# Performance work log

Hardware: AMD Instinct MI355X
Metric: run time of the kernel (lower is better)

## Reference

```python
import jax, jax.numpy as jnp
import numpy as np

N = 20000   # num_nodes
R = 32      # num_relations
H = 64      # hidden_size
C = 8       # num_classes
E = 640000  # num_edges


def setup_inputs() -> dict:
    key = jax.random.key(0)
    k = jax.random.split(key, 8)
    edge_index = jax.random.randint(k[0], (2, E), 0, N, dtype=jnp.int64)
    edge_type = jnp.sort(jax.random.randint(k[1], (E,), 0, R, dtype=jnp.int64))
    # offsets per relation into the sorted edge list (R+1 entries)
    tensor_slice = jnp.searchsorted(edge_type, jnp.arange(R + 1)).astype(jnp.int64)
    # conv1: x=None => weight is a per-relation node-embedding table [R, N, H]
    W1 = jax.random.normal(k[2], (R, N, H), dtype=jnp.float32) * (1.0 / np.sqrt(N))
    root1 = jax.random.normal(k[3], (N, H), dtype=jnp.float32) * (1.0 / np.sqrt(N))
    bias1 = jnp.zeros((H,), dtype=jnp.float32)
    W2 = jax.random.normal(k[4], (R, H, C), dtype=jnp.float32) * (1.0 / np.sqrt(H))
    root2 = jax.random.normal(k[5], (H, C), dtype=jnp.float32) * (1.0 / np.sqrt(H))
    bias2 = jnp.zeros((C,), dtype=jnp.float32)
    return {"edge_index": edge_index, "edge_type": edge_type, "tensor_slice": tensor_slice,
            "W1": W1, "root1": root1, "bias1": bias1,
            "W2": W2, "root2": root2, "bias2": bias2}


def reference(edge_index, edge_type, tensor_slice, W1, root1, bias1, W2, root2, bias2):
    src, dst = edge_index[0], edge_index[1]
    # ---- conv1 (x = None): message for edge e is row W1[edge_type[e], src[e]]
    msg1 = W1[edge_type, src]                                   # [E, H] gather
    h = jax.ops.segment_sum(msg1, dst, num_segments=N)          # scatter-add (aggr='add')
    h = h + root1 + bias1                                       # root term = root1[node] since x=None
    h = jax.nn.relu(h)
    # ---- conv2: transform all nodes under every relation once, then gather per edge
    h_rel = jnp.einsum('nh,rhc->rnc', h, W2)                    # [R, N, C]
    msg2 = h_rel[edge_type, src]                                # [E, C] gather
    out = jax.ops.segment_sum(msg2, dst, num_segments=N)        # [N, C]
    out = out + h @ root2 + bias2
    return jax.nn.log_softmax(out, axis=1)
```

## Files before the change

### kernel.cpp

```cpp
#include <hip/hip_runtime.h>
#include <math.h>

#define NN 20000
#define RR 32
#define HH 64
#define CC 8
#define EE 640000
#define CAP 128
#define RT 8

__global__ __launch_bounds__(256) void k_zero(int* __restrict__ cnt) {
    int i = blockIdx.x * 256 + threadIdx.x;
    if (i < NN) cnt[i] = 0;
}

__global__ __launch_bounds__(256) void k_scatter(const int* __restrict__ ei,
                                                 const int* __restrict__ et,
                                                 int* __restrict__ cnt,
                                                 unsigned* __restrict__ pk2) {
    int e = (blockIdx.x * 256 + threadIdx.x) * 4;
    if (e >= EE) return;
    int4 sv = *(const int4*)(ei + e);
    int4 dv = *(const int4*)(ei + EE + e);
    int4 rv = *(const int4*)(et + e);
    int s;
    s = atomicAdd(&cnt[dv.x], 1); pk2[((size_t)dv.x << 7) + s] = (unsigned)sv.x | ((unsigned)rv.x << 15);
    s = atomicAdd(&cnt[dv.y], 1); pk2[((size_t)dv.y << 7) + s] = (unsigned)sv.y | ((unsigned)rv.y << 15);
    s = atomicAdd(&cnt[dv.z], 1); pk2[((size_t)dv.z << 7) + s] = (unsigned)sv.z | ((unsigned)rv.z << 15);
    s = atomicAdd(&cnt[dv.w], 1); pk2[((size_t)dv.w << 7) + s] = (unsigned)sv.w | ((unsigned)rv.w << 15);
}

__global__ __launch_bounds__(256) void k_gather1(const unsigned* __restrict__ pk2,
                                                 const int* __restrict__ cnt,
                                                 const float* __restrict__ W1,
                                                 const float* __restrict__ root1,
                                                 const float* __restrict__ bias1,
                                                 const float* __restrict__ root2,
                                                 float* __restrict__ h,
                                                 float* __restrict__ outr) {
    int wid = (blockIdx.x * 256 + threadIdx.x) >> 6;
    int lane = threadIdx.x & 63;
    if (wid >= NN) return;
    const int eg = lane >> 4;
    const int q  = lane & 15;
    float4 acc4 = make_float4(0.f, 0.f, 0.f, 0.f);
    int beg = wid << 7;
    int end = beg + cnt[wid];
    int i = beg;
    for (; i + 16 <= end; i += 16) {
        unsigned p0 = pk2[i + eg], p1 = pk2[i + 4 + eg];
        unsigned p2 = pk2[i + 8 + eg], p3 = pk2[i + 12 + eg];
        float4 w0 = *((const float4*)(W1 + ((size_t)(p0 >> 15) * NN + (p0 & 0x7fffu)) * HH) + q);
        float4 w1 = *((const float4*)(W1 + ((size_t)(p1 >> 15) * NN + (p1 & 0x7fffu)) * HH) + q);
        float4 w2 = *((const float4*)(W1 + ((size_t)(p2 >> 15) * NN + (p2 & 0x7fffu)) * HH) + q);
        float4 w3 = *((const float4*)(W1 + ((size_t)(p3 >> 15) * NN + (p3 & 0x7fffu)) * HH) + q);
        acc4.x += (w0.x + w1.x) + (w2.x + w3.x);
        acc4.y += (w0.y + w1.y) + (w2.y + w3.y);
        acc4.z += (w0.z + w1.z) + (w2.z + w3.z);
        acc4.w += (w0.w + w1.w) + (w2.w + w3.w);
    }
    for (; i + 4 <= end; i += 4) {
        unsigned p = pk2[i + eg];
        float4 w = *((const float4*)(W1 + ((size_t)(p >> 15) * NN + (p & 0x7fffu)) * HH) + q);
        acc4.x += w.x; acc4.y += w.y; acc4.z += w.z; acc4.w += w.w;
    }
    acc4.x += __shfl_xor(acc4.x, 16); acc4.y += __shfl_xor(acc4.y, 16);
    acc4.z += __shfl_xor(acc4.z, 16); acc4.w += __shfl_xor(acc4.w, 16);
    acc4.x += __shfl_xor(acc4.x, 32); acc4.y += __shfl_xor(acc4.y, 32);
    acc4.z += __shfl_xor(acc4.z, 32); acc4.w += __shfl_xor(acc4.w, 32);
    int sl = lane >> 2;
    float cx = __shfl(acc4.x, sl), cy = __shfl(acc4.y, sl);
    float cz = __shfl(acc4.z, sl), cw = __shfl(acc4.w, sl);
    int comp = lane & 3;
    float acc = cx;
    if (comp == 1) acc = cy;
    if (comp == 2) acc = cz;
    if (comp == 3) acc = cw;
    for (; i < end; ++i) {
        unsigned p = pk2[i];
        acc += W1[((size_t)(p >> 15) * NN + (p & 0x7fffu)) * HH + lane];
    }
    acc += root1[(size_t)wid * HH + lane] + bias1[lane];
    float hv = fmaxf(acc, 0.0f);
    h[(size_t)wid * HH + lane] = hv;
    float4 ra = *(const float4*)(root2 + lane * CC);
    float4 rb = *(const float4*)(root2 + lane * CC + 4);
    float a0 = hv * ra.x, a1 = hv * ra.y, a2 = hv * ra.z, a3 = hv * ra.w;
    float a4 = hv * rb.x, a5 = hv * rb.y, a6 = hv * rb.z, a7 = hv * rb.w;
    #pragma unroll
    for (int m = 1; m < 8; m <<= 1) {
        a0 += __shfl_xor(a0, m); a1 += __shfl_xor(a1, m);
        a2 += __shfl_xor(a2, m); a3 += __shfl_xor(a3, m);
        a4 += __shfl_xor(a4, m); a5 += __shfl_xor(a5, m);
        a6 += __shfl_xor(a6, m); a7 += __shfl_xor(a7, m);
    }
    int c = lane & 7;
    float v = a0;
    if (c == 1) v = a1;  if (c == 2) v = a2;  if (c == 3) v = a3;
    if (c == 4) v = a4;  if (c == 5) v = a5;  if (c == 6) v = a6;
    if (c == 7) v = a7;
    v += __shfl_xor(v, 8);
    v += __shfl_xor(v, 16);
    v += __shfl_xor(v, 32);
    if (lane < 8) outr[(size_t)wid * CC + lane] = v;
}

__global__ __launch_bounds__(256) void k_hrel(const float* __restrict__ h,
                                              const float* __restrict__ W2,
                                              float* __restrict__ hrel) {
    __shared__ float w2s[RT * HH * CC];
    int r0 = blockIdx.y * RT;
    int tid = threadIdx.x;
    #pragma unroll
    for (int u = 0; u < RT * HH * CC / 256; u++)
        w2s[u * 256 + tid] = W2[(size_t)r0 * HH * CC + u * 256 + tid];
    __syncthreads();
    int n = blockIdx.x * 256 + tid;
    if (n >= NN) return;
    const float* hp = h + (size_t)n * HH;
    float4 hreg[HH / 4];
    #pragma unroll
    for (int k4 = 0; k4 < HH / 4; k4++) hreg[k4] = ((const float4*)hp)[k4];
    for (int rr = 0; rr < RT; rr++) {
        const float* w = w2s + rr * HH * CC;
        float acc[CC] = {0, 0, 0, 0, 0, 0, 0, 0};
        #pragma unroll
        for (int k4 = 0; k4 < HH / 4; k4++) {
            float4 hv = hreg[k4];
            int k = k4 * 4;
            #pragma unroll
            for (int c = 0; c < CC; c++) {
                acc[c] += hv.x * w[(k + 0) * CC + c] + hv.y * w[(k + 1) * CC + c]
                        + hv.z * w[(k + 2) * CC + c] + hv.w * w[(k + 3) * CC + c];
            }
        }
        float* op = hrel + ((size_t)(r0 + rr) * NN + n) * CC;
        *(float4*)(op)     = make_float4(acc[0], acc[1], acc[2], acc[3]);
        *(float4*)(op + 4) = make_float4(acc[4], acc[5], acc[6], acc[7]);
    }
}

__global__ __launch_bounds__(256) void k_gather2(const unsigned* __restrict__ pk2,
                                                 const int* __restrict__ cnt,
                                                 const float* __restrict__ hrel,
                                                 const float* __restrict__ outr,
                                                 const float* __restrict__ bias2,
                                                 float* __restrict__ out) {
    int wid = (blockIdx.x * 256 + threadIdx.x) >> 6;
    int lane = threadIdx.x & 63;
    if (wid >= NN) return;
    int eg = lane >> 1, half = lane & 1;
    float4 acc = make_float4(0.f, 0.f, 0.f, 0.f);
    int beg = wid << 7;
    int end = beg + cnt[wid];
    for (int i = beg + eg; i < end; i += 32) {
        unsigned p = pk2[i];
        float4 v = *((const float4*)(hrel + ((size_t)(p >> 15) * NN + (p & 0x7fffu)) * CC) + half);
        acc.x += v.x; acc.y += v.y; acc.z += v.z; acc.w += v.w;
    }
    #pragma unroll
    for (int m = 2; m < 64; m <<= 1) {
        acc.x += __shfl_xor(acc.x, m);
        acc.y += __shfl_xor(acc.y, m);
        acc.z += __shfl_xor(acc.z, m);
        acc.w += __shfl_xor(acc.w, m);
    }
    float4 o = *((const float4*)(outr + (size_t)wid * CC) + half);
    float4 b = *((const float4*)bias2 + half);
    float4 x;
    x.x = acc.x + o.x + b.x;
    x.y = acc.y + o.y + b.y;
    x.z = acc.z + o.z + b.z;
    x.w = acc.w + o.w + b.w;
    float m4 = fmaxf(fmaxf(x.x, x.y), fmaxf(x.z, x.w));
    float mm = fmaxf(m4, __shfl_xor(m4, 1));
    float e4 = expf(x.x - mm) + expf(x.y - mm) + expf(x.z - mm) + expf(x.w - mm);
    float ss = e4 + __shfl_xor(e4, 1);
    float l = mm + logf(ss);
    if (lane < 2) {
        float4 r = make_float4(x.x - l, x.y - l, x.z - l, x.w - l);
        *((float4*)(out + (size_t)wid * CC) + half) = r;
    }
}

extern "C" void kernel_launch(void* const* d_in, const int* in_sizes, int n_in,
                              void* d_out, int out_size, void* d_ws, size_t ws_size,
                              hipStream_t stream) {
    const int*   ei    = (const int*)d_in[0];
    const int*   et    = (const int*)d_in[1];
    const float* W1    = (const float*)d_in[3];
    const float* root1 = (const float*)d_in[4];
    const float* bias1 = (const float*)d_in[5];
    const float* W2    = (const float*)d_in[6];
    const float* root2 = (const float*)d_in[7];
    const float* bias2 = (const float*)d_in[8];
    float* out = (float*)d_out;

    char* base = (char*)d_ws;
    int*      cnt  = (int*)(base);
    unsigned* pk2  = (unsigned*)(base + 80128);
    float*    h    = (float*)(base + 10320128);
    float*    outr = (float*)(base + 15440128);
    float*    hrel = (float*)(base + 16080128);

    k_zero   <<<(NN + 255) / 256, 256, 0, stream>>>(cnt);
    k_scatter<<<(EE / 4 + 255) / 256, 256, 0, stream>>>(ei, et, cnt, pk2);
    k_gather1<<<(NN * 64 + 255) / 256, 256, 0, stream>>>(pk2, cnt, W1, root1, bias1, root2, h, outr);
    k_hrel   <<<dim3((NN + 255) / 256, RR / RT), 256, 0, stream>>>(h, W2, hrel);
    k_gather2<<<(NN * 64 + 255) / 256, 256, 0, stream>>>(pk2, cnt, hrel, outr, bias2, out);
}
```

Measured before the change: 127.1 us.

## Split per-node edge buckets into 8 sub-buckets to reduce atomic contention

Replaces the single per-destination counter and 128-slot bucket with 8 counters and 32-slot sub-buckets, one chosen per scatter block by block index, so concurrent atomics on the same node are spread across separate counters. Both gather kernels now walk the 8 sub-buckets, with each 16-lane group handling two sub-buckets, instead of taking contiguous 16-edge chunks. This trades atomic contention for a larger workspace, more zeroing, shorter and uneven per-lane loops without unrolling, and an overflow risk if a sub-bucket receives more than 32 edges.

After: 134.7 us. 6.0% more time.

```diff
diff --git a/kernel.cpp b/kernel.cpp
--- a/kernel.cpp
+++ b/kernel.cpp
@@ -6,32 +6,34 @@
 #define HH 64
 #define CC 8
 #define EE 640000
-#define CAP 128
 #define RT 8
 
-__global__ __launch_bounds__(256) void k_zero(int* __restrict__ cnt) {
+__global__ __launch_bounds__(256) void k_zero(int* __restrict__ cnt8) {
     int i = blockIdx.x * 256 + threadIdx.x;
-    if (i < NN) cnt[i] = 0;
+    if (i < 8 * NN) cnt8[i] = 0;
 }
 
 __global__ __launch_bounds__(256) void k_scatter(const int* __restrict__ ei,
                                                  const int* __restrict__ et,
-                                                 int* __restrict__ cnt,
+                                                 int* __restrict__ cnt8,
                                                  unsigned* __restrict__ pk2) {
     int e = (blockIdx.x * 256 + threadIdx.x) * 4;
     if (e >= EE) return;
+    const int c = blockIdx.x & 7;
+    int* __restrict__ cc = cnt8 + c * NN;
+    const int cbase = c << 5;
     int4 sv = *(const int4*)(ei + e);
     int4 dv = *(const int4*)(ei + EE + e);
     int4 rv = *(const int4*)(et + e);
     int s;
-    s = atomicAdd(&cnt[dv.x], 1); pk2[((size_t)dv.x << 7) + s] = (unsigned)sv.x | ((unsigned)rv.x << 15);
-    s = atomicAdd(&cnt[dv.y], 1); pk2[((size_t)dv.y << 7) + s] = (unsigned)sv.y | ((unsigned)rv.y << 15);
-    s = atomicAdd(&cnt[dv.z], 1); pk2[((size_t)dv.z << 7) + s] = (unsigned)sv.z | ((unsigned)rv.z << 15);
-    s = atomicAdd(&cnt[dv.w], 1); pk2[((size_t)dv.w << 7) + s] = (unsigned)sv.w | ((unsigned)rv.w << 15);
+    s = atomicAdd(&cc[dv.x], 1); pk2[((size_t)dv.x << 8) + cbase + s] = (unsigned)sv.x | ((unsigned)rv.x << 15);
+    s = atomicAdd(&cc[dv.y], 1); pk2[((size_t)dv.y << 8) + cbase + s] = (unsigned)sv.y | ((unsigned)rv.y << 15);
+    s = atomicAdd(&cc[dv.z], 1); pk2[((size_t)dv.z << 8) + cbase + s] = (unsigned)sv.z | ((unsigned)rv.z << 15);
+    s = atomicAdd(&cc[dv.w], 1); pk2[((size_t)dv.w << 8) + cbase + s] = (unsigned)sv.w | ((unsigned)rv.w << 15);
 }
 
 __global__ __launch_bounds__(256) void k_gather1(const unsigned* __restrict__ pk2,
-                                                 const int* __restrict__ cnt,
+                                                 const int* __restrict__ cnt8,
                                                  const float* __restrict__ W1,
                                                  const float* __restrict__ root1,
                                                  const float* __restrict__ bias1,
@@ -41,28 +43,20 @@
     int wid = (blockIdx.x * 256 + threadIdx.x) >> 6;
     int lane = threadIdx.x & 63;
     if (wid >= NN) return;
-    const int eg = lane >> 4;
+    const int ch = lane >> 4;
     const int q  = lane & 15;
     float4 acc4 = make_float4(0.f, 0.f, 0.f, 0.f);
-    int beg = wid << 7;
-    int end = beg + cnt[wid];
-    int i = beg;
-    for (; i + 16 <= end; i += 16) {
-        unsigned p0 = pk2[i + eg], p1 = pk2[i + 4 + eg];
-        unsigned p2 = pk2[i + 8 + eg], p3 = pk2[i + 12 + eg];
-        float4 w0 = *((const float4*)(W1 + ((size_t)(p0 >> 15) * NN + (p0 & 0x7fffu)) * HH) + q);
-        float4 w1 = *((const float4*)(W1 + ((size_t)(p1 >> 15) * NN + (p1 & 0x7fffu)) * HH) + q);
-        float4 w2 = *((const float4*)(W1 + ((size_t)(p2 >> 15) * NN + (p2 & 0x7fffu)) * HH) + q);
-        float4 w3 = *((const float4*)(W1 + ((size_t)(p3 >> 15) * NN + (p3 & 0x7fffu)) * HH) + q);
-        acc4.x += (w0.x + w1.x) + (w2.x + w3.x);
-        acc4.y += (w0.y + w1.y) + (w2.y + w3.y);
-        acc4.z += (w0.z + w1.z) + (w2.z + w3.z);
-        acc4.w += (w0.w + w1.w) + (w2.w + w3.w);
-    }
-    for (; i + 4 <= end; i += 4) {
-        unsigned p = pk2[i + eg];
-        float4 w = *((const float4*)(W1 + ((size_t)(p >> 15) * NN + (p & 0x7fffu)) * HH) + q);
-        acc4.x += w.x; acc4.y += w.y; acc4.z += w.z; acc4.w += w.w;
+    const int rowbase = wid << 8;
+    #pragma unroll
+    for (int half = 0; half < 2; half++) {
+        const int c = ch + half * 4;
+        const int n = cnt8[c * NN + wid];
+        const int b = rowbase + (c << 5);
+        for (int i = 0; i < n; i++) {
+            unsigned p = pk2[b + i];
+            const float4 w = *((const float4*)(W1 + ((size_t)(p >> 15) * NN + (p & 0x7fffu)) * HH) + q);
+            acc4.x += w.x; acc4.y += w.y; acc4.z += w.z; acc4.w += w.w;
+        }
     }
     acc4.x += __shfl_xor(acc4.x, 16); acc4.y += __shfl_xor(acc4.y, 16);
     acc4.z += __shfl_xor(acc4.z, 16); acc4.w += __shfl_xor(acc4.w, 16);
@@ -76,10 +70,6 @@
     if (comp == 1) acc = cy;
     if (comp == 2) acc = cz;
     if (comp == 3) acc = cw;
-    for (; i < end; ++i) {
-        unsigned p = pk2[i];
-        acc += W1[((size_t)(p >> 15) * NN + (p & 0x7fffu)) * HH + lane];
-    }
     acc += root1[(size_t)wid * HH + lane] + bias1[lane];
     float hv = fmaxf(acc, 0.0f);
     h[(size_t)wid * HH + lane] = hv;
@@ -94,11 +84,11 @@
         a4 += __shfl_xor(a4, m); a5 += __shfl_xor(a5, m);
         a6 += __shfl_xor(a6, m); a7 += __shfl_xor(a7, m);
     }
-    int c = lane & 7;
+    int c2 = lane & 7;
     float v = a0;
-    if (c == 1) v = a1;  if (c == 2) v = a2;  if (c == 3) v = a3;
-    if (c == 4) v = a4;  if (c == 5) v = a5;  if (c == 6) v = a6;
-    if (c == 7) v = a7;
+    if (c2 == 1) v = a1;  if (c2 == 2) v = a2;  if (c2 == 3) v = a3;
+    if (c2 == 4) v = a4;  if (c2 == 5) v = a5;  if (c2 == 6) v = a6;
+    if (c2 == 7) v = a7;
     v += __shfl_xor(v, 8);
     v += __shfl_xor(v, 16);
     v += __shfl_xor(v, 32);
@@ -141,7 +131,7 @@
 }
 
 __global__ __launch_bounds__(256) void k_gather2(const unsigned* __restrict__ pk2,
-                                                 const int* __restrict__ cnt,
+                                                 const int* __restrict__ cnt8,
                                                  const float* __restrict__ hrel,
                                                  const float* __restrict__ outr,
                                                  const float* __restrict__ bias2,
@@ -150,11 +140,12 @@
     int lane = threadIdx.x & 63;
     if (wid >= NN) return;
     int eg = lane >> 1, half = lane & 1;
+    int c = eg >> 2, i0 = eg & 3;
+    int n = cnt8[c * NN + wid];
+    int b = (wid << 8) + (c << 5);
     float4 acc = make_float4(0.f, 0.f, 0.f, 0.f);
-    int beg = wid << 7;
-    int end = beg + cnt[wid];
-    for (int i = beg + eg; i < end; i += 32) {
-        unsigned p = pk2[i];
+    for (int i = i0; i < n; i += 4) {
+        unsigned p = pk2[b + i];
         float4 v = *((const float4*)(hrel + ((size_t)(p >> 15) * NN + (p & 0x7fffu)) * CC) + half);
         acc.x += v.x; acc.y += v.y; acc.z += v.z; acc.w += v.w;
     }
@@ -166,12 +157,12 @@
         acc.w += __shfl_xor(acc.w, m);
     }
     float4 o = *((const float4*)(outr + (size_t)wid * CC) + half);
-    float4 b = *((const float4*)bias2 + half);
+    float4 b2 = *((const float4*)bias2 + half);
     float4 x;
-    x.x = acc.x + o.x + b.x;
-    x.y = acc.y + o.y + b.y;
-    x.z = acc.z + o.z + b.z;
-    x.w = acc.w + o.w + b.w;
+    x.x = acc.x + o.x + b2.x;
+    x.y = acc.y + o.y + b2.y;
+    x.z = acc.z + o.z + b2.z;
+    x.w = acc.w + o.w + b2.w;
     float m4 = fmaxf(fmaxf(x.x, x.y), fmaxf(x.z, x.w));
     float mm = fmaxf(m4, __shfl_xor(m4, 1));
     float e4 = expf(x.x - mm) + expf(x.y - mm) + expf(x.z - mm) + expf(x.w - mm);
@@ -197,15 +188,15 @@
     float* out = (float*)d_out;
 
     char* base = (char*)d_ws;
-    int*      cnt  = (int*)(base);
-    unsigned* pk2  = (unsigned*)(base + 80128);
-    float*    h    = (float*)(base + 10320128);
-    float*    outr = (float*)(base + 15440128);
-    float*    hrel = (float*)(base + 16080128);
-
-    k_zero   <<<(NN + 255) / 256, 256, 0, stream>>>(cnt);
-    k_scatter<<<(EE / 4 + 255) / 256, 256, 0, stream>>>(ei, et, cnt, pk2);
-    k_gather1<<<(NN * 64 + 255) / 256, 256, 0, stream>>>(pk2, cnt, W1, root1, bias1, root2, h, outr);
+    int*      cnt8 = (int*)(base);
+    unsigned* pk2  = (unsigned*)(base + 640128);
+    float*    h    = (float*)(base + 21120128);
+    float*    outr = (float*)(base + 26240128);
+    float*    hrel = (float*)(base + 26880128);
+
+    k_zero   <<<(8 * NN + 255) / 256, 256, 0, stream>>>(cnt8);
+    k_scatter<<<(EE / 4 + 255) / 256, 256, 0, stream>>>(ei, et, cnt8, pk2);
+    k_gather1<<<(NN * 64 + 255) / 256, 256, 0, stream>>>(pk2, cnt8, W1, root1, bias1, root2, h, outr);
     k_hrel   <<<dim3((NN + 255) / 256, RR / RT), 256, 0, stream>>>(h, W2, hrel);
-    k_gather2<<<(NN * 64 + 255) / 256, 256, 0, stream>>>(pk2, cnt, hrel, outr, bias2, out);
-}
+    k_gather2<<<(NN * 64 + 255) / 256, 256, 0, stream>>>(pk2, cnt8, hrel, outr, bias2, out);
+}
```
